# Optimization experiments

Measured on AMD Instinct MI355X. Metric: run time of the kernel, lower is better.

The kernel has to match this reference:

```python
import jax, jax.numpy as jnp
import numpy as np
from jax import lax

B, CIN, COUT, K, H, W = 32, 64, 64, 3, 160, 160
STRIDE, PAD = 1, 1


def setup_inputs() -> dict:
    key = jax.random.key(0)
    kx, kw = jax.random.split(key)
    x = jax.random.normal(kx, (B, CIN, H, W), dtype=jnp.float32)
    # xavier_normal-ish init for the full-precision weight [Cout, Cin, K, K]
    fan_in, fan_out = CIN * K * K, COUT * K * K
    std = float(np.sqrt(2.0 / (fan_in + fan_out)))
    w = jax.random.normal(kw, (COUT, CIN, K, K), dtype=jnp.float32) * std
    return {"x": x, "w": w}


def reference(x, w):
    # Binarize activations: sign (bi_act_method=0)
    xb = jnp.sign(x)
    # Weight path (bi_w_scale=2): clamp to [-1,1], per-output-channel |w| mean scale
    wc = jnp.clip(w, -1.0, 1.0)
    mean_val = jnp.mean(jnp.abs(wc), axis=(1, 2, 3), keepdims=True)  # [Cout,1,1,1]
    bw = jnp.sign(wc) * mean_val
    # conv2d, NCHW / OIHW
    out = lax.conv_general_dilated(
        xb, bw,
        window_strides=(STRIDE, STRIDE),
        padding=((PAD, PAD), (PAD, PAD)),
        dimension_numbers=("NCHW", "OIHW", "NCHW"),
    )
    return out
```

## Files before the change

### kernel.cpp

```cpp
#include <hip/hip_runtime.h>
#include <cstdint>

#define WID   160
#define HEI   160
#define HWPIX (WID * HEI)
#define CIN_  64
#define COUT_ 64
#define BATCH 32
#define PW    162
#define PPIX  (PW * PW)
#define NBORDER 636

__global__ __launch_bounds__(64) void wprep_kernel(const float* __restrict__ w,
                                                   uint64_t* __restrict__ wpack,
                                                   float* __restrict__ alpha) {
    const int co = blockIdx.x;
    const int ci = threadIdx.x;
    const float* wp = w + ((size_t)co * CIN_ + ci) * 9;

    float vals[9];
    float s = 0.0f;
#pragma unroll
    for (int t = 0; t < 9; ++t) {
        float v = wp[t];
        vals[t] = v;
        s += fminf(fabsf(v), 1.0f);
    }
#pragma unroll
    for (int t = 0; t < 9; ++t) {
        unsigned long long m = __ballot(vals[t] > 0.0f);
        if (ci == 0) wpack[co * 9 + t] = m;
    }
#pragma unroll
    for (int off = 32; off > 0; off >>= 1) s += __shfl_down(s, off);
    if (ci == 0) alpha[co] = s * (1.0f / 576.0f);
}

__global__ __launch_bounds__(256) void binpack_kernel(const float* __restrict__ x,
                                                      uint64_t* __restrict__ packed) {
    const int t  = blockIdx.x * 256 + threadIdx.x;
    const int b  = blockIdx.y;
    const int p4 = t * 4;
    const int y  = p4 / WID;
    const int x0 = p4 - y * WID;
    const float4* xp = (const float4*)(x + (size_t)b * CIN_ * HWPIX + p4);

    uint32_t lo[4] = {0, 0, 0, 0}, hi[4] = {0, 0, 0, 0};
#pragma unroll
    for (int ci = 0; ci < 32; ++ci) {
        float4 v = xp[(size_t)ci * (HWPIX / 4)];
        lo[0] |= (uint32_t)(v.x > 0.0f) << ci;
        lo[1] |= (uint32_t)(v.y > 0.0f) << ci;
        lo[2] |= (uint32_t)(v.z > 0.0f) << ci;
        lo[3] |= (uint32_t)(v.w > 0.0f) << ci;
    }
#pragma unroll
    for (int ci = 0; ci < 32; ++ci) {
        float4 v = xp[(size_t)(ci + 32) * (HWPIX / 4)];
        hi[0] |= (uint32_t)(v.x > 0.0f) << ci;
        hi[1] |= (uint32_t)(v.y > 0.0f) << ci;
        hi[2] |= (uint32_t)(v.z > 0.0f) << ci;
        hi[3] |= (uint32_t)(v.w > 0.0f) << ci;
    }
    uint64_t* dst = packed + (size_t)b * PPIX + (size_t)(y + 1) * PW + (x0 + 1);
#pragma unroll
    for (int i = 0; i < 4; ++i)
        dst[i] = ((uint64_t)hi[i] << 32) | lo[i];
}

__global__ __launch_bounds__(256) void conv_kernel(const uint64_t* __restrict__ packed,
                                                   const uint64_t* __restrict__ wpack,
                                                   const float* __restrict__ alpha,
                                                   float* __restrict__ out) {
    const int t4 = blockIdx.x * 256 + threadIdx.x;
    const int b  = blockIdx.y;
    const int p0 = t4 * 4;
    const int y  = p0 / WID;
    const int x  = p0 - y * WID;
    const uint64_t* pb = packed + (size_t)b * PPIX + (size_t)y * PW + x;

    uint64_t p[3][6];
#pragma unroll
    for (int ky = 0; ky < 3; ++ky)
#pragma unroll
        for (int kx = 0; kx < 6; ++kx)
            p[ky][kx] = pb[(size_t)ky * PW + kx];

    float* op = out + (size_t)b * COUT_ * HWPIX + p0;
#pragma unroll 4
    for (int co = 0; co < COUT_; ++co) {
        const uint64_t* wp = wpack + co * 9;
        int pc0 = 0, pc1 = 0, pc2 = 0, pc3 = 0;
#pragma unroll
        for (int ky = 0; ky < 3; ++ky)
#pragma unroll
            for (int kx = 0; kx < 3; ++kx) {
                const uint64_t ww = wp[ky * 3 + kx];
                pc0 += __popcll(p[ky][kx + 0] ^ ww);
                pc1 += __popcll(p[ky][kx + 1] ^ ww);
                pc2 += __popcll(p[ky][kx + 2] ^ ww);
                pc3 += __popcll(p[ky][kx + 3] ^ ww);
            }
        const float a = alpha[co];
        const float c = 576.0f * a;
        const float m = -2.0f * a;
        float4 r;
        r.x = fmaf((float)pc0, m, c);
        r.y = fmaf((float)pc1, m, c);
        r.z = fmaf((float)pc2, m, c);
        r.w = fmaf((float)pc3, m, c);
        *(float4*)(op + (size_t)co * HWPIX) = r;
    }
}

__global__ __launch_bounds__(256) void fixup_kernel(const uint64_t* __restrict__ packed,
                                                    const uint64_t* __restrict__ wpack,
                                                    const float* __restrict__ alpha,
                                                    float* __restrict__ out) {
    const int t = blockIdx.x * 256 + threadIdx.x;
    if (t >= NBORDER * BATCH) return;
    const int b = t / NBORDER;
    const int i = t - b * NBORDER;
    int x, y;
    if      (i < 160) { y = 0;       x = i;       }
    else if (i < 320) { y = 159;     x = i - 160; }
    else if (i < 478) { x = 0;       y = i - 319; }
    else              { x = 159;     y = i - 477; }

    const uint64_t* pb = packed + (size_t)b * PPIX + (size_t)y * PW + x;
    uint64_t p[9];
    int valid[9];
    int nv = 0;
#pragma unroll
    for (int ky = 0; ky < 3; ++ky)
#pragma unroll
        for (int kx = 0; kx < 3; ++kx) {
            const int yy = y + ky - 1, xx = x + kx - 1;
            const int v = (yy >= 0) && (yy < HEI) && (xx >= 0) && (xx < WID);
            valid[ky * 3 + kx] = v;
            nv += v;
            p[ky * 3 + kx] = pb[(size_t)ky * PW + kx];
        }
    float* op = out + (size_t)b * COUT_ * HWPIX + (size_t)y * WID + x;
    for (int co = 0; co < COUT_; ++co) {
        int pc = 0;
#pragma unroll
        for (int tt = 0; tt < 9; ++tt)
            pc += valid[tt] ? __popcll(p[tt] ^ wpack[co * 9 + tt]) : 0;
        op[(size_t)co * HWPIX] = alpha[co] * (float)((nv << 6) - 2 * pc);
    }
}

extern "C" void kernel_launch(void* const* d_in, const int* in_sizes, int n_in,
                              void* d_out, int out_size, void* d_ws, size_t ws_size,
                              hipStream_t stream) {
    const float* x = (const float*)d_in[0];
    const float* w = (const float*)d_in[1];
    float* out = (float*)d_out;

    uint64_t* wpack  = (uint64_t*)d_ws;
    float*    alpha  = (float*)((char*)d_ws + 4608);
    uint64_t* packed = (uint64_t*)((char*)d_ws + 8192);

    hipMemsetAsync(packed, 0, (size_t)BATCH * PPIX * sizeof(uint64_t), stream);

    wprep_kernel<<<dim3(COUT_), dim3(64), 0, stream>>>(w, wpack, alpha);
    binpack_kernel<<<dim3(HWPIX / 4 / 256, BATCH), dim3(256), 0, stream>>>(x, packed);
    conv_kernel<<<dim3(HWPIX / 4 / 256, BATCH), dim3(256), 0, stream>>>(packed, wpack, alpha, out);
    fixup_kernel<<<dim3((NBORDER * BATCH + 255) / 256), dim3(256), 0, stream>>>(packed, wpack, alpha, out);
}
```

Measured before the change: 457.5 us.

## Fuse binarize-pack into conv kernel with LDS row tiles and halo

Merges the binarize/pack kernel and the popcount conv kernel into one. Each block packs an 8-row tile plus a 1-row halo from x into shared memory, then runs the XOR-popcount conv from LDS instead of re-reading the packed buffer from global memory. The packed interior rows are still written to global for the border fixup kernel, and the memset of the padded buffer is dropped because the fixup kernel masks out-of-range taps. The cost is that halo rows of x are read and packed twice (about 25% extra x reads), and the grid is smaller with larger 320-thread blocks.

```diff
diff --git a/kernel.cpp b/kernel.cpp
--- a/kernel.cpp
+++ b/kernel.cpp
@@ -10,6 +10,8 @@
 #define PW    162
 #define PPIX  (PW * PW)
 #define NBORDER 636
+#define TR    8
+#define TLROWS (TR + 2)
 
 __global__ __launch_bounds__(64) void wprep_kernel(const float* __restrict__ w,
                                                    uint64_t* __restrict__ wpack,
@@ -36,57 +38,73 @@
     if (ci == 0) alpha[co] = s * (1.0f / 576.0f);
 }
 
-__global__ __launch_bounds__(256) void binpack_kernel(const float* __restrict__ x,
-                                                      uint64_t* __restrict__ packed) {
-    const int t  = blockIdx.x * 256 + threadIdx.x;
-    const int b  = blockIdx.y;
-    const int p4 = t * 4;
-    const int y  = p4 / WID;
-    const int x0 = p4 - y * WID;
-    const float4* xp = (const float4*)(x + (size_t)b * CIN_ * HWPIX + p4);
+__global__ __launch_bounds__(320) void bconv_kernel(const float* __restrict__ x,
+                                                    const uint64_t* __restrict__ wpack,
+                                                    const float* __restrict__ alpha,
+                                                    uint64_t* __restrict__ packed,
+                                                    float* __restrict__ out) {
+    __shared__ uint64_t lds[TLROWS][PW];
+    const int tid = threadIdx.x;
+    const int b   = blockIdx.y;
+    const int y0  = blockIdx.x * TR;
 
-    uint32_t lo[4] = {0, 0, 0, 0}, hi[4] = {0, 0, 0, 0};
+    for (int i = tid; i < TLROWS * PW; i += 320)
+        ((uint64_t*)lds)[i] = 0;
+    __syncthreads();
+
+    for (int g = tid; g < TLROWS * 40; g += 320) {
+        const int rr = g / 40;
+        const int yy = y0 + rr - 1;
+        if (yy >= 0 && yy < HEI) {
+            const int x4 = (g - rr * 40) * 4;
+            const float4* xp = (const float4*)(x + (size_t)b * CIN_ * HWPIX
+                                                 + (size_t)yy * WID + x4);
+            uint32_t lo[4] = {0, 0, 0, 0}, hi[4] = {0, 0, 0, 0};
 #pragma unroll
-    for (int ci = 0; ci < 32; ++ci) {
-        float4 v = xp[(size_t)ci * (HWPIX / 4)];
-        lo[0] |= (uint32_t)(v.x > 0.0f) << ci;
-        lo[1] |= (uint32_t)(v.y > 0.0f) << ci;
-        lo[2] |= (uint32_t)(v.z > 0.0f) << ci;
-        lo[3] |= (uint32_t)(v.w > 0.0f) << ci;
+            for (int ci = 0; ci < 32; ++ci) {
+                float4 v = xp[(size_t)ci * (HWPIX / 4)];
+                lo[0] |= (uint32_t)(v.x > 0.0f) << ci;
+                lo[1] |= (uint32_t)(v.y > 0.0f) << ci;
+                lo[2] |= (uint32_t)(v.z > 0.0f) << ci;
+                lo[3] |= (uint32_t)(v.w > 0.0f) << ci;
+            }
+#pragma unroll
+            for (int ci = 0; ci < 32; ++ci) {
+                float4 v = xp[(size_t)(ci + 32) * (HWPIX / 4)];
+                hi[0] |= (uint32_t)(v.x > 0.0f) << ci;
+                hi[1] |= (uint32_t)(v.y > 0.0f) << ci;
+                hi[2] |= (uint32_t)(v.z > 0.0f) << ci;
+                hi[3] |= (uint32_t)(v.w > 0.0f) << ci;
+            }
+            uint64_t w4[4];
+#pragma unroll
+            for (int i = 0; i < 4; ++i)
+                w4[i] = ((uint64_t)hi[i] << 32) | lo[i];
+#pragma unroll
+            for (int i = 0; i < 4; ++i)
+                lds[rr][x4 + 1 + i] = w4[i];
+            if (rr >= 1 && rr <= TR) {
+                uint64_t* dst = packed + (size_t)b * PPIX
+                              + (size_t)(yy + 1) * PW + (x4 + 1);
+#pragma unroll
+                for (int i = 0; i < 4; ++i) dst[i] = w4[i];
+            }
+        }
     }
-#pragma unroll
-    for (int ci = 0; ci < 32; ++ci) {
-        float4 v = xp[(size_t)(ci + 32) * (HWPIX / 4)];
-        hi[0] |= (uint32_t)(v.x > 0.0f) << ci;
-        hi[1] |= (uint32_t)(v.y > 0.0f) << ci;
-        hi[2] |= (uint32_t)(v.z > 0.0f) << ci;
-        hi[3] |= (uint32_t)(v.w > 0.0f) << ci;
-    }
-    uint64_t* dst = packed + (size_t)b * PPIX + (size_t)(y + 1) * PW + (x0 + 1);
-#pragma unroll
-    for (int i = 0; i < 4; ++i)
-        dst[i] = ((uint64_t)hi[i] << 32) | lo[i];
-}
+    __syncthreads();
 
-__global__ __launch_bounds__(256) void conv_kernel(const uint64_t* __restrict__ packed,
-                                                   const uint64_t* __restrict__ wpack,
-                                                   const float* __restrict__ alpha,
-                                                   float* __restrict__ out) {
-    const int t4 = blockIdx.x * 256 + threadIdx.x;
-    const int b  = blockIdx.y;
-    const int p0 = t4 * 4;
-    const int y  = p0 / WID;
-    const int x  = p0 - y * WID;
-    const uint64_t* pb = packed + (size_t)b * PPIX + (size_t)y * PW + x;
+    const int r  = tid / 40;
+    const int x4 = (tid - r * 40) * 4;
+    const int y  = y0 + r;
 
     uint64_t p[3][6];
 #pragma unroll
     for (int ky = 0; ky < 3; ++ky)
 #pragma unroll
         for (int kx = 0; kx < 6; ++kx)
-            p[ky][kx] = pb[(size_t)ky * PW + kx];
+            p[ky][kx] = lds[r + ky][x4 + kx];
 
-    float* op = out + (size_t)b * COUT_ * HWPIX + p0;
+    float* op = out + (size_t)b * COUT_ * HWPIX + (size_t)y * WID + x4;
 #pragma unroll 4
     for (int co = 0; co < COUT_; ++co) {
         const uint64_t* wp = wpack + co * 9;
@@ -104,12 +122,12 @@
         const float a = alpha[co];
         const float c = 576.0f * a;
         const float m = -2.0f * a;
-        float4 r;
-        r.x = fmaf((float)pc0, m, c);
-        r.y = fmaf((float)pc1, m, c);
-        r.z = fmaf((float)pc2, m, c);
-        r.w = fmaf((float)pc3, m, c);
-        *(float4*)(op + (size_t)co * HWPIX) = r;
+        float4 rv;
+        rv.x = fmaf((float)pc0, m, c);
+        rv.y = fmaf((float)pc1, m, c);
+        rv.z = fmaf((float)pc2, m, c);
+        rv.w = fmaf((float)pc3, m, c);
+        *(float4*)(op + (size_t)co * HWPIX) = rv;
     }
 }
 
@@ -162,10 +180,8 @@
     float*    alpha  = (float*)((char*)d_ws + 4608);
     uint64_t* packed = (uint64_t*)((char*)d_ws + 8192);
 
-    hipMemsetAsync(packed, 0, (size_t)BATCH * PPIX * sizeof(uint64_t), stream);
 
     wprep_kernel<<<dim3(COUT_), dim3(64), 0, stream>>>(w, wpack, alpha);
-    binpack_kernel<<<dim3(HWPIX / 4 / 256, BATCH), dim3(256), 0, stream>>>(x, packed);
-    conv_kernel<<<dim3(HWPIX / 4 / 256, BATCH), dim3(256), 0, stream>>>(packed, wpack, alpha, out);
+    bconv_kernel<<<dim3(HEI / TR, BATCH), dim3(320), 0, stream>>>(x, wpack, alpha, packed, out);
     fixup_kernel<<<dim3((NBORDER * BATCH + 255) / 256), dim3(256), 0, stream>>>(packed, wpack, alpha, out);
 }
```

Result: slower. 611.5 us (+33.7%).

## Fuse weight prep into binpack, merge border fixup into conv, drop memset

Applied to the files above, without the earlier changes.

Weight packing now runs in an extra x-block (index 25) of the activation binpack kernel. The border fixup moves into the conv kernel: interior threads cover only columns 4..155 of rows 1..158, and dedicated threads handle border pixels four at a time. The interior path no longer reads the padded halo and the border path masks invalid taps, so the memset of the padded buffer is removed. This cuts launches from four kernels plus a memset to two, at the risk of a slow tail from the serial border threads inside the conv grid.

```diff
diff --git a/kernel.cpp b/kernel.cpp
--- a/kernel.cpp
+++ b/kernel.cpp
@@ -9,35 +9,40 @@
 #define BATCH 32
 #define PW    162
 #define PPIX  (PW * PW)
-#define NBORDER 636
+#define NINT   6004
+#define BSTART 6016
+#define NBORD  396
 
-__global__ __launch_bounds__(64) void wprep_kernel(const float* __restrict__ w,
+__global__ __launch_bounds__(256) void prep_kernel(const float* __restrict__ x,
+                                                   const float* __restrict__ w,
+                                                   uint64_t* __restrict__ packed,
                                                    uint64_t* __restrict__ wpack,
                                                    float* __restrict__ alpha) {
-    const int co = blockIdx.x;
-    const int ci = threadIdx.x;
-    const float* wp = w + ((size_t)co * CIN_ + ci) * 9;
+    if (blockIdx.x == 25) {
+        if (blockIdx.y >= 16) return;
+        const int wv = threadIdx.x >> 6;
+        const int ci = threadIdx.x & 63;
+        const int co = blockIdx.y * 4 + wv;
+        const float* wp = w + ((size_t)co * CIN_ + ci) * 9;
+        float vals[9];
+        float s = 0.0f;
+#pragma unroll
+        for (int t = 0; t < 9; ++t) {
+            float v = wp[t];
+            vals[t] = v;
+            s += fminf(fabsf(v), 1.0f);
+        }
+#pragma unroll
+        for (int t = 0; t < 9; ++t) {
+            unsigned long long m = __ballot(vals[t] > 0.0f);
+            if (ci == 0) wpack[co * 9 + t] = m;
+        }
+#pragma unroll
+        for (int off = 32; off > 0; off >>= 1) s += __shfl_down(s, off);
+        if (ci == 0) alpha[co] = s * (1.0f / 576.0f);
+        return;
+    }
 
-    float vals[9];
-    float s = 0.0f;
-#pragma unroll
-    for (int t = 0; t < 9; ++t) {
-        float v = wp[t];
-        vals[t] = v;
-        s += fminf(fabsf(v), 1.0f);
-    }
-#pragma unroll
-    for (int t = 0; t < 9; ++t) {
-        unsigned long long m = __ballot(vals[t] > 0.0f);
-        if (ci == 0) wpack[co * 9 + t] = m;
-    }
-#pragma unroll
-    for (int off = 32; off > 0; off >>= 1) s += __shfl_down(s, off);
-    if (ci == 0) alpha[co] = s * (1.0f / 576.0f);
-}
-
-__global__ __launch_bounds__(256) void binpack_kernel(const float* __restrict__ x,
-                                                      uint64_t* __restrict__ packed) {
     const int t  = blockIdx.x * 256 + threadIdx.x;
     const int b  = blockIdx.y;
     const int p4 = t * 4;
@@ -72,82 +77,87 @@
                                                    const uint64_t* __restrict__ wpack,
                                                    const float* __restrict__ alpha,
                                                    float* __restrict__ out) {
-    const int t4 = blockIdx.x * 256 + threadIdx.x;
-    const int b  = blockIdx.y;
-    const int p0 = t4 * 4;
-    const int y  = p0 / WID;
-    const int x  = p0 - y * WID;
-    const uint64_t* pb = packed + (size_t)b * PPIX + (size_t)y * PW + x;
+    const int t = blockIdx.x * 256 + threadIdx.x;
+    const int b = blockIdx.y;
+    const uint64_t* pimg = packed + (size_t)b * PPIX;
+    float* oimg = out + (size_t)b * COUT_ * HWPIX;
 
-    uint64_t p[3][6];
-#pragma unroll
-    for (int ky = 0; ky < 3; ++ky)
-#pragma unroll
-        for (int kx = 0; kx < 6; ++kx)
-            p[ky][kx] = pb[(size_t)ky * PW + kx];
+    if (t < NINT) {
+        const int r = t / 38;
+        const int c = t - r * 38;
+        const int y = r + 1;
+        const int x = (c + 1) * 4;
+        const uint64_t* pb = pimg + (size_t)y * PW + x;
 
-    float* op = out + (size_t)b * COUT_ * HWPIX + p0;
-#pragma unroll 4
-    for (int co = 0; co < COUT_; ++co) {
-        const uint64_t* wp = wpack + co * 9;
-        int pc0 = 0, pc1 = 0, pc2 = 0, pc3 = 0;
+        uint64_t p[3][6];
 #pragma unroll
         for (int ky = 0; ky < 3; ++ky)
 #pragma unroll
-            for (int kx = 0; kx < 3; ++kx) {
-                const uint64_t ww = wp[ky * 3 + kx];
-                pc0 += __popcll(p[ky][kx + 0] ^ ww);
-                pc1 += __popcll(p[ky][kx + 1] ^ ww);
-                pc2 += __popcll(p[ky][kx + 2] ^ ww);
-                pc3 += __popcll(p[ky][kx + 3] ^ ww);
+            for (int kx = 0; kx < 6; ++kx)
+                p[ky][kx] = pb[(size_t)ky * PW + kx];
+
+        float* op = oimg + (size_t)y * WID + x;
+#pragma unroll 4
+        for (int co = 0; co < COUT_; ++co) {
+            const uint64_t* wp = wpack + co * 9;
+            int pc0 = 0, pc1 = 0, pc2 = 0, pc3 = 0;
+#pragma unroll
+            for (int ky = 0; ky < 3; ++ky)
+#pragma unroll
+                for (int kx = 0; kx < 3; ++kx) {
+                    const uint64_t ww = wp[ky * 3 + kx];
+                    pc0 += __popcll(p[ky][kx + 0] ^ ww);
+                    pc1 += __popcll(p[ky][kx + 1] ^ ww);
+                    pc2 += __popcll(p[ky][kx + 2] ^ ww);
+                    pc3 += __popcll(p[ky][kx + 3] ^ ww);
+                }
+            const float a = alpha[co];
+            const float cc = 576.0f * a;
+            const float m  = -2.0f * a;
+            float4 rv;
+            rv.x = fmaf((float)pc0, m, cc);
+            rv.y = fmaf((float)pc1, m, cc);
+            rv.z = fmaf((float)pc2, m, cc);
+            rv.w = fmaf((float)pc3, m, cc);
+            *(float4*)(op + (size_t)co * HWPIX) = rv;
+        }
+    } else if (t >= BSTART && t < BSTART + NBORD) {
+        const int i = t - BSTART;
+        int y, x4;
+        if      (i < 40) { y = 0;   x4 = i * 4;        }
+        else if (i < 80) { y = 159; x4 = (i - 40) * 4; }
+        else {
+            const int j = i - 80;
+            y  = 1 + (j >> 1);
+            x4 = (j & 1) * 156;
+        }
+#pragma unroll 1
+        for (int px = 0; px < 4; ++px) {
+            const int x = x4 + px;
+            const uint64_t* pb = pimg + (size_t)y * PW + x;
+            uint64_t p[9];
+            int valid[9];
+            int nv = 0;
+#pragma unroll
+            for (int ky = 0; ky < 3; ++ky)
+#pragma unroll
+                for (int kx = 0; kx < 3; ++kx) {
+                    const int yy = y + ky - 1, xx = x + kx - 1;
+                    const int v = (yy >= 0) && (yy < HEI) && (xx >= 0) && (xx < WID);
+                    valid[ky * 3 + kx] = v;
+                    nv += v;
+                    p[ky * 3 + kx] = pb[(size_t)ky * PW + kx];
+                }
+            float* op = oimg + (size_t)y * WID + x;
+            for (int co = 0; co < COUT_; ++co) {
+                const uint64_t* wp = wpack + co * 9;
+                int pc = 0;
+#pragma unroll
+                for (int tt = 0; tt < 9; ++tt)
+                    pc += valid[tt] ? __popcll(p[tt] ^ wp[tt]) : 0;
+                op[(size_t)co * HWPIX] = alpha[co] * (float)((nv << 6) - 2 * pc);
             }
-        const float a = alpha[co];
-        const float c = 576.0f * a;
-        const float m = -2.0f * a;
-        float4 r;
-        r.x = fmaf((float)pc0, m, c);
-        r.y = fmaf((float)pc1, m, c);
-        r.z = fmaf((float)pc2, m, c);
-        r.w = fmaf((float)pc3, m, c);
-        *(float4*)(op + (size_t)co * HWPIX) = r;
-    }
-}
-
-__global__ __launch_bounds__(256) void fixup_kernel(const uint64_t* __restrict__ packed,
-                                                    const uint64_t* __restrict__ wpack,
-                                                    const float* __restrict__ alpha,
-                                                    float* __restrict__ out) {
-    const int t = blockIdx.x * 256 + threadIdx.x;
-    if (t >= NBORDER * BATCH) return;
-    const int b = t / NBORDER;
-    const int i = t - b * NBORDER;
-    int x, y;
-    if      (i < 160) { y = 0;       x = i;       }
-    else if (i < 320) { y = 159;     x = i - 160; }
-    else if (i < 478) { x = 0;       y = i - 319; }
-    else              { x = 159;     y = i - 477; }
-
-    const uint64_t* pb = packed + (size_t)b * PPIX + (size_t)y * PW + x;
-    uint64_t p[9];
-    int valid[9];
-    int nv = 0;
-#pragma unroll
-    for (int ky = 0; ky < 3; ++ky)
-#pragma unroll
-        for (int kx = 0; kx < 3; ++kx) {
-            const int yy = y + ky - 1, xx = x + kx - 1;
-            const int v = (yy >= 0) && (yy < HEI) && (xx >= 0) && (xx < WID);
-            valid[ky * 3 + kx] = v;
-            nv += v;
-            p[ky * 3 + kx] = pb[(size_t)ky * PW + kx];
         }
-    float* op = out + (size_t)b * COUT_ * HWPIX + (size_t)y * WID + x;
-    for (int co = 0; co < COUT_; ++co) {
-        int pc = 0;
-#pragma unroll
-        for (int tt = 0; tt < 9; ++tt)
-            pc += valid[tt] ? __popcll(p[tt] ^ wpack[co * 9 + tt]) : 0;
-        op[(size_t)co * HWPIX] = alpha[co] * (float)((nv << 6) - 2 * pc);
     }
 }
 
@@ -162,10 +172,7 @@
     float*    alpha  = (float*)((char*)d_ws + 4608);
     uint64_t* packed = (uint64_t*)((char*)d_ws + 8192);
 
-    hipMemsetAsync(packed, 0, (size_t)BATCH * PPIX * sizeof(uint64_t), stream);
 
-    wprep_kernel<<<dim3(COUT_), dim3(64), 0, stream>>>(w, wpack, alpha);
-    binpack_kernel<<<dim3(HWPIX / 4 / 256, BATCH), dim3(256), 0, stream>>>(x, packed);
-    conv_kernel<<<dim3(HWPIX / 4 / 256, BATCH), dim3(256), 0, stream>>>(packed, wpack, alpha, out);
-    fixup_kernel<<<dim3((NBORDER * BATCH + 255) / 256), dim3(256), 0, stream>>>(packed, wpack, alpha, out);
+    prep_kernel<<<dim3(26, BATCH), dim3(256), 0, stream>>>(x, w, packed, wpack, alpha);
+    conv_kernel<<<dim3(26, BATCH), dim3(256), 0, stream>>>(packed, wpack, alpha, out);
 }
```

After: 493.1 us. +7.8%, slower.
